# Optimization experiments

Measured on AMD Instinct MI355X. Metric: run time of the kernel, lower is better.

## Reference

```python
import jax, jax.numpy as jnp
import numpy as np

EPS = 1e-6

def _layernorm(x, g, b):
    m = jnp.mean(x, axis=-1, keepdims=True)
    v = jnp.var(x, axis=-1, keepdims=True)
    return (x - m) / jnp.sqrt(v + EPS) * g + b

def setup_inputs() -> dict:
    key = jax.random.key(0)
    ks = jax.random.split(key, 12)
    B, L, D, H = 2, 1024, 1024, 16
    s = 0.02  # weight init scale
    return {
        "query": jax.random.normal(ks[0], (B, L, D), jnp.float32),
        "pos_bias": jax.random.normal(ks[1], (H, L, L), jnp.float32) * 0.1,
        "postag_bias": jax.random.normal(ks[2], (B, H, L, L), jnp.float32) * 0.1,
        "lex_mask": jax.random.normal(ks[3], (B, L), jnp.float32) * 0.1,
        "mask": jax.random.randint(ks[4], (B, L), 0, 2).astype(jnp.int32),
        "Wq": jax.random.normal(ks[5], (D, D), jnp.float32) * s,
        "bq": jnp.zeros((D,), jnp.float32),
        "Wk": jax.random.normal(ks[6], (D, D), jnp.float32) * s,
        "bk": jnp.zeros((D,), jnp.float32),
        "Wv": jax.random.normal(ks[7], (D, D), jnp.float32) * s,
        "bv": jnp.zeros((D,), jnp.float32),
        "Wo": jax.random.normal(ks[8], (D, D), jnp.float32) * s,
        "bo": jnp.zeros((D,), jnp.float32),
        "gamma": jnp.ones((D,), jnp.float32),
        "beta": jnp.zeros((D,), jnp.float32),
    }

def reference(query, pos_bias, postag_bias, lex_mask, mask,
              Wq, bq, Wk, bk, Wv, bv, Wo, bo, gamma, beta):
    B, L, D = query.shape
    H = pos_bias.shape[0]
    dk = D // H
    scale = jnp.asarray(dk ** 0.5, query.dtype)

    residual = query
    context = query              # context=None path: set BEFORE pre-LN norm
    qn = _layernorm(query, gamma, beta)  # pre_ln=True applies only to query

    Q = (qn @ Wq.T + bq).reshape(B, L, H, dk)       # bqhd
    K = (context @ Wk.T + bk).reshape(B, L, H, dk)  # bkhd
    V = (context @ Wv.T + bv).reshape(B, L, H, dk)

    # (B,H,L,S) logits with all additive bias terms
    logits = jnp.einsum('bqhd,bkhd->bhqk', Q, K) / scale
    logits = logits + pos_bias[None]               # rel-pos bias (H,L,S)
    logits = logits + postag_bias                  # POS-tag bias (B,H,L,S)
    logits = logits + lex_mask[:, None, None, :]   # additive lexical mask
    logits = jnp.where(mask[:, None, None, :] == 0, -jnp.inf, logits)

    attn = jax.nn.softmax(logits, axis=-1)         # dropout inactive (eval)
    out = jnp.einsum('bhqk,bkhd->bqhd', attn, V).reshape(B, L, D)
    out = out @ Wo.T + bo
    out = out + residual
    return out, attn
```

## Files before the change

### kernel.cpp

```cpp
#include <hip/hip_runtime.h>
#include <hip/hip_bf16.h>
#include <math.h>

constexpr int B = 2, L = 1024, D = 1024, H = 16, DK = 64;
constexpr int M = B * L;
constexpr int DD = D * D;

typedef __attribute__((ext_vector_type(8))) short bf16x8;
typedef __attribute__((ext_vector_type(4))) float f32x4;

#define SB0() __builtin_amdgcn_sched_barrier(0)

__device__ inline unsigned short f2bf(float f) {
    __hip_bfloat16 h = __float2bfloat16(f);
    return __builtin_bit_cast(unsigned short, h);
}

__device__ inline void glds16(const void* g, void* l) {
    __builtin_amdgcn_global_load_lds((const __attribute__((address_space(1))) void*)g,
                                     (__attribute__((address_space(3))) void*)l,
                                     16, 0, 0);
}

__global__ __launch_bounds__(256) void ln2_kernel(const float* __restrict__ x,
                                                  const float* __restrict__ gamma,
                                                  const float* __restrict__ beta,
                                                  const float* __restrict__ lex,
                                                  const int* __restrict__ mask,
                                                  unsigned short* __restrict__ qn16,
                                                  unsigned short* __restrict__ q16,
                                                  float* __restrict__ lsmout) {
    int row = blockIdx.x;
    int t = threadIdx.x;
    if (t == 0) lsmout[row] = mask[row] ? lex[row] : -1e30f;
    const float4 v = ((const float4*)(x + (size_t)row * D))[t];
    float s  = v.x + v.y + v.z + v.w;
    float sq = v.x*v.x + v.y*v.y + v.z*v.z + v.w*v.w;
    #pragma unroll
    for (int m = 32; m >= 1; m >>= 1) {
        s  += __shfl_xor(s, m, 64);
        sq += __shfl_xor(sq, m, 64);
    }
    __shared__ float rs[4], rq[4];
    int wid = t >> 6;
    if ((t & 63) == 0) { rs[wid] = s; rq[wid] = sq; }
    __syncthreads();
    s  = rs[0] + rs[1] + rs[2] + rs[3];
    sq = rq[0] + rq[1] + rq[2] + rq[3];
    float mean = s * (1.0f / D);
    float var  = sq * (1.0f / D) - mean * mean;
    float rstd = rsqrtf(var + 1e-6f);
    float4 g  = ((const float4*)gamma)[t];
    float4 bb = ((const float4*)beta)[t];
    ushort4 on, oq;
    on.x = f2bf((v.x - mean) * rstd * g.x + bb.x);
    on.y = f2bf((v.y - mean) * rstd * g.y + bb.y);
    on.z = f2bf((v.z - mean) * rstd * g.z + bb.z);
    on.w = f2bf((v.w - mean) * rstd * g.w + bb.w);
    oq.x = f2bf(v.x); oq.y = f2bf(v.y); oq.z = f2bf(v.z); oq.w = f2bf(v.w);
    ((ushort4*)(qn16 + (size_t)row * D))[t] = on;
    ((ushort4*)(q16  + (size_t)row * D))[t] = oq;
}

__global__ __launch_bounds__(256) void wconv_kernel(const float* __restrict__ Wq,
                                                    const float* __restrict__ Wk,
                                                    const float* __restrict__ Wv,
                                                    const float* __restrict__ Wo,
                                                    unsigned short* __restrict__ out) {
    const float* src = (blockIdx.y == 0) ? Wq : (blockIdx.y == 1) ? Wk
                       : (blockIdx.y == 2) ? Wv : Wo;
    size_t i = (size_t)blockIdx.x * 256 + threadIdx.x;
    float4 v = ((const float4*)src)[i];
    ushort4 o;
    o.x = f2bf(v.x); o.y = f2bf(v.y); o.z = f2bf(v.z); o.w = f2bf(v.w);
    ((ushort4*)(out + (size_t)blockIdx.y * DD))[i] = o;
}

__global__ __launch_bounds__(256) void gemm_qkv(
        const unsigned short* __restrict__ qn16, const unsigned short* __restrict__ q16,
        const unsigned short* __restrict__ W,
        const float* __restrict__ bq, const float* __restrict__ bk,
        const float* __restrict__ bv,
        unsigned short* __restrict__ Qm, unsigned short* __restrict__ Km,
        unsigned short* __restrict__ Vm) {
    __shared__ __align__(16) unsigned short As[128 * 64];
    __shared__ __align__(16) unsigned short Ws[128 * 64];
    int t = threadIdx.x, lane = t & 63, w = t >> 6;
    int quad = lane >> 4, l15 = lane & 15;
    int nt = blockIdx.x;
    int bm = blockIdx.y * 128;
    const unsigned short* A = (nt < 8) ? qn16 : q16;
    const float* bias = (nt < 8) ? bq : ((nt < 16) ? bk : bv);
    unsigned short* Cout = (nt < 8) ? Qm : ((nt < 16) ? Km : Vm);
    int bn_local = (nt & 7) * 128;
    int wm = (w >> 1) * 64, wn = (w & 1) * 64;
    f32x4 acc[4][4] = {};
    for (int k0 = 0; k0 < D; k0 += 64) {
        __syncthreads();
        const unsigned short* ap = A + (size_t)(bm + w * 32) * D + k0;
        const unsigned short* wp = W + (size_t)(nt * 128 + w * 32) * D + k0;
        #pragma unroll
        for (int i = 0; i < 4; i++) {
            int c = i * 64 + lane;
            int r = c >> 3, g = (c & 7) ^ (r & 7);
            glds16(ap + (size_t)r * D + g * 8, &As[w * 2048 + i * 512]);
            glds16(wp + (size_t)r * D + g * 8, &Ws[w * 2048 + i * 512]);
        }
        __syncthreads();
        #pragma unroll
        for (int k2 = 0; k2 < 2; k2++) {
            bf16x8 av[4], bw[4];
            #pragma unroll
            for (int i = 0; i < 4; i++) {
                int r = wm + i * 16 + l15;
                av[i] = *(const bf16x8*)&As[r * 64 + (((quad + 4 * k2) ^ (r & 7)) * 8)];
            }
            #pragma unroll
            for (int j = 0; j < 4; j++) {
                int r = wn + j * 16 + l15;
                bw[j] = *(const bf16x8*)&Ws[r * 64 + (((quad + 4 * k2) ^ (r & 7)) * 8)];
            }
            #pragma unroll
            for (int i = 0; i < 4; i++)
                #pragma unroll
                for (int j = 0; j < 4; j++)
                    acc[i][j] = __builtin_amdgcn_mfma_f32_16x16x32_bf16(av[i], bw[j], acc[i][j], 0, 0, 0);
        }
    }
    #pragma unroll
    for (int j = 0; j < 4; j++) {
        int col = bn_local + wn + j * 16 + l15;
        float bcol = bias[col];
        #pragma unroll
        for (int i = 0; i < 4; i++)
            #pragma unroll
            for (int rg = 0; rg < 4; rg++) {
                int row = bm + wm + i * 16 + quad * 4 + rg;
                Cout[(size_t)row * D + col] = f2bf(acc[i][j][rg] + bcol);
            }
    }
}

__global__ __launch_bounds__(256) void vtrans_kernel(const unsigned short* __restrict__ Vm,
                                                     unsigned short* __restrict__ Vt) {
    __shared__ unsigned short sb[128 * 66];
    int t = threadIdx.x;
    int z = blockIdx.y;
    int b = z >> 4, h = z & 15;
    int s0 = blockIdx.x * 128;
    size_t base = (size_t)b * L * D + (size_t)h * 64;
    #pragma unroll
    for (int i = 0; i < 4; i++) {
        int idx = t + 256 * i;
        int r = idx >> 3, c8 = idx & 7;
        uint4 vv = *(const uint4*)&Vm[base + (size_t)(s0 + r) * D + c8 * 8];
        unsigned int* sp = (unsigned int*)&sb[r * 66 + c8 * 8];
        sp[0] = vv.x; sp[1] = vv.y; sp[2] = vv.z; sp[3] = vv.w;
    }
    __syncthreads();
    #pragma unroll
    for (int i = 0; i < 4; i++) {
        int idx = t + 256 * i;
        int d = idx >> 4, sc = idx & 15;
        unsigned short tmp[8];
        #pragma unroll
        for (int j = 0; j < 8; j++) tmp[j] = sb[(sc * 8 + j) * 66 + d];
        *(uint4*)&Vt[((size_t)z * 64 + d) * L + s0 + sc * 8] = *(uint4*)tmp;
    }
}

__global__ __launch_bounds__(256, 2) void attn_pv_kernel(
        const unsigned short* __restrict__ Qm, const unsigned short* __restrict__ Km,
        const unsigned short* __restrict__ Vt,
        const float* __restrict__ pos_bias, const float* __restrict__ postag,
        const float* __restrict__ lsm, float* __restrict__ attn_out,
        unsigned short* __restrict__ ctx16) {
    __shared__ __align__(16) unsigned short pool[32768];
    __shared__ __align__(16) unsigned short p_sh[16][136];
    __shared__ __align__(16) unsigned short q_sh[16][72];
    __shared__ float lsm_sh[1024];
    __shared__ float redA[16][4], redB[16][4];

    int t = threadIdx.x, lane = t & 63, w = t >> 6;
    int quad = lane >> 4, l15 = lane & 15;
    int qt = blockIdx.x & 63;
    int bh = blockIdx.x >> 6;
    int b = bh >> 4, h = bh & 15;
    int q0 = qt * 16;
    int q = q0 + l15;
    size_t base = (size_t)b * L * D + (size_t)h * DK;

    if (t < 128) {
        int r = t >> 3, c8 = t & 7;
        *(uint4*)&q_sh[r][c8 * 8] = *(const uint4*)&Qm[base + (size_t)(q0 + r) * D + c8 * 8];
    }
    ((float4*)lsm_sh)[t] = ((const float4*)(lsm + b * L))[t];
    __syncthreads();
    bf16x8 qb0 = *(const bf16x8*)&q_sh[l15][quad * 8];
    bf16x8 qb1 = *(const bf16x8*)&q_sh[l15][32 + quad * 8];

    const float* pbQ = pos_bias + ((size_t)h * L + q0) * L;
    const float* ptQ = postag + ((size_t)bh * L + q0) * L;

    f32x4 acc[16] = {};
    SB0();
    {
        const unsigned short* kpn = Km + base + (size_t)(w * 32) * D;
        #pragma unroll
        for (int i = 0; i < 4; i++) {
            int r = i * 8 + (lane >> 3);
            int g = (lane & 7) ^ (r & 7);
            glds16(kpn + (size_t)r * D + g * 8, &pool[w * 2048 + i * 512]);
        }
    }
    SB0();
    {
        int rb = lane >> 3;
        int gb = (lane & 7) ^ rb;
        #pragma unroll
        for (int i = 0; i < 2; i++) {
            glds16(pbQ + (size_t)(i * 8 + rb) * L + w * 32 + gb * 4,
                   &pool[16384 + w * 2048 + i * 512]);
            glds16(ptQ + (size_t)(i * 8 + rb) * L + w * 32 + gb * 4,
                   &pool[16384 + w * 2048 + 1024 + i * 512]);
        }
    }
    SB0();
    #pragma unroll
    for (int st = 0; st < 8; st++) {
        int bc = st & 1, bn = bc ^ 1;
        if (st < 7) {
            SB0();
            const unsigned short* kpn = Km + base + (size_t)((st + 1) * 128 + w * 32) * D;
            #pragma unroll
            for (int i = 0; i < 4; i++) {
                int r = i * 8 + (lane >> 3);
                int g = (lane & 7) ^ (r & 7);
                glds16(kpn + (size_t)r * D + g * 8, &pool[bn * 8192 + w * 2048 + i * 512]);
            }
            SB0();
            {
                int rb = lane >> 3;
                int gb = (lane & 7) ^ rb;
                #pragma unroll
                for (int i = 0; i < 2; i++) {
                    glds16(pbQ + (size_t)(i * 8 + rb) * L + (st + 1) * 128 + w * 32 + gb * 4,
                           &pool[16384 + bn * 8192 + w * 2048 + i * 512]);
                    glds16(ptQ + (size_t)(i * 8 + rb) * L + (st + 1) * 128 + w * 32 + gb * 4,
                           &pool[16384 + bn * 8192 + w * 2048 + 1024 + i * 512]);
                }
            }
            SB0();
            asm volatile("s_waitcnt vmcnt(8)" ::: "memory");
        } else {
            SB0();
            asm volatile("s_waitcnt vmcnt(0)" ::: "memory");
        }
        SB0();
        int r7 = l15 & 7;
        const unsigned short* kB = &pool[bc * 8192 + w * 2048];
        bf16x8 ka00 = *(const bf16x8*)&kB[l15 * 64 + ((quad ^ r7) * 8)];
        bf16x8 ka01 = *(const bf16x8*)&kB[l15 * 64 + (((quad + 4) ^ r7) * 8)];
        bf16x8 ka10 = *(const bf16x8*)&kB[(16 + l15) * 64 + ((quad ^ r7) * 8)];
        bf16x8 ka11 = *(const bf16x8*)&kB[(16 + l15) * 64 + (((quad + 4) ^ r7) * 8)];
        const float* pbL = (const float*)&pool[16384 + bc * 8192 + w * 2048];
        const float* ptL = (const float*)&pool[16384 + bc * 8192 + w * 2048 + 1024];
        float4 pb0 = *(const float4*)&pbL[l15 * 32 + ((quad ^ r7) * 4)];
        float4 pb1 = *(const float4*)&pbL[l15 * 32 + (((quad + 4) ^ r7) * 4)];
        float4 pt0 = *(const float4*)&ptL[l15 * 32 + ((quad ^ r7) * 4)];
        float4 pt1 = *(const float4*)&ptL[l15 * 32 + (((quad + 4) ^ r7) * 4)];
        int s_u0 = st * 128 + w * 32 + quad * 4;
        float4 l0 = *(const float4*)&lsm_sh[s_u0];
        float4 l1 = *(const float4*)&lsm_sh[s_u0 + 16];
        int ti0 = 2 * st, ti1 = ti0 + 1;
        acc[ti0] = __builtin_amdgcn_mfma_f32_16x16x32_bf16(ka00, qb0, acc[ti0], 0, 0, 0);
        acc[ti0] = __builtin_amdgcn_mfma_f32_16x16x32_bf16(ka01, qb1, acc[ti0], 0, 0, 0);
        acc[ti1] = __builtin_amdgcn_mfma_f32_16x16x32_bf16(ka10, qb0, acc[ti1], 0, 0, 0);
        acc[ti1] = __builtin_amdgcn_mfma_f32_16x16x32_bf16(ka11, qb1, acc[ti1], 0, 0, 0);
        acc[ti0][0] = acc[ti0][0] * 0.125f + (pb0.x + pt0.x + l0.x);
        acc[ti0][1] = acc[ti0][1] * 0.125f + (pb0.y + pt0.y + l0.y);
        acc[ti0][2] = acc[ti0][2] * 0.125f + (pb0.z + pt0.z + l0.z);
        acc[ti0][3] = acc[ti0][3] * 0.125f + (pb0.w + pt0.w + l0.w);
        acc[ti1][0] = acc[ti1][0] * 0.125f + (pb1.x + pt1.x + l1.x);
        acc[ti1][1] = acc[ti1][1] * 0.125f + (pb1.y + pt1.y + l1.y);
        acc[ti1][2] = acc[ti1][2] * 0.125f + (pb1.z + pt1.z + l1.z);
        acc[ti1][3] = acc[ti1][3] * 0.125f + (pb1.w + pt1.w + l1.w);
    }
    float mx = -1e30f;
    #pragma unroll
    for (int ti = 0; ti < 16; ti++)
        #pragma unroll
        for (int rg = 0; rg < 4; rg++) mx = fmaxf(mx, acc[ti][rg]);
    mx = fmaxf(mx, __shfl_xor(mx, 16, 64));
    mx = fmaxf(mx, __shfl_xor(mx, 32, 64));
    if (quad == 0) redA[l15][w] = mx;
    __syncthreads();
    mx = fmaxf(fmaxf(redA[l15][0], redA[l15][1]), fmaxf(redA[l15][2], redA[l15][3]));
    float sum = 0.f;
    #pragma unroll
    for (int ti = 0; ti < 16; ti++)
        #pragma unroll
        for (int rg = 0; rg < 4; rg++) {
            float e = __expf(acc[ti][rg] - mx);
            acc[ti][rg] = e;
            sum += e;
        }
    sum += __shfl_xor(sum, 16, 64);
    sum += __shfl_xor(sum, 32, 64);
    if (quad == 0) redB[l15][w] = sum;
    __syncthreads();
    float inv = 1.0f / (redB[l15][0] + redB[l15][1] + redB[l15][2] + redB[l15][3]);
    #pragma unroll
    for (int ti = 0; ti < 16; ti++) {
        int s0 = (ti >> 1) * 128 + w * 32 + (ti & 1) * 16 + quad * 4;
        float4 o;
        o.x = acc[ti][0] * inv; o.y = acc[ti][1] * inv;
        o.z = acc[ti][2] * inv; o.w = acc[ti][3] * inv;
        acc[ti][0] = o.x; acc[ti][1] = o.y; acc[ti][2] = o.z; acc[ti][3] = o.w;
        *(float4*)&attn_out[((size_t)bh * L + q) * L + s0] = o;
    }
    f32x4 cacc = {};
    const unsigned short* vbase = Vt + ((size_t)bh * 64 + w * 16) * L;
    SB0();
    #pragma unroll
    for (int i = 0; i < 4; i++) {
        int r = i * 4 + (lane >> 4);
        int g = (lane & 15) ^ (r & 7);
        glds16(vbase + (size_t)r * L + g * 8, &pool[w * 2048 + i * 512]);
    }
    SB0();
    #pragma unroll
    for (int st = 0; st < 8; st++) {
        int bc = st & 1;
        #pragma unroll
        for (int u = 0; u < 2; u++) {
            f32x4 p = acc[2 * st + u];
            ushort4 pu;
            pu.x = f2bf(p[0]); pu.y = f2bf(p[1]); pu.z = f2bf(p[2]); pu.w = f2bf(p[3]);
            *(ushort4*)&p_sh[l15][w * 32 + u * 16 + quad * 4] = pu;
        }
        if (st < 7) {
            SB0();
            #pragma unroll
            for (int i = 0; i < 4; i++) {
                int r = i * 4 + (lane >> 4);
                int g = (lane & 15) ^ (r & 7);
                glds16(vbase + (size_t)r * L + (st + 1) * 128 + g * 8,
                       &pool[(bc ^ 1) * 8192 + w * 2048 + i * 512]);
            }
            SB0();
            asm volatile("s_waitcnt vmcnt(4)" ::: "memory");
        } else {
            SB0();
            asm volatile("s_waitcnt vmcnt(0)" ::: "memory");
        }
        asm volatile("s_waitcnt lgkmcnt(0)" ::: "memory");
        SB0();
        __builtin_amdgcn_s_barrier();
        SB0();
        const unsigned short* vB = &pool[bc * 8192 + w * 2048];
        #pragma unroll
        for (int kk = 0; kk < 4; kk++) {
            bf16x8 vf = *(const bf16x8*)&vB[l15 * 128 + (((kk * 4 + quad) ^ (l15 & 7)) * 8)];
            bf16x8 pf = *(const bf16x8*)&p_sh[l15][kk * 32 + quad * 8];
            cacc = __builtin_amdgcn_mfma_f32_16x16x32_bf16(pf, vf, cacc, 0, 0, 0);
        }
        SB0();
        __builtin_amdgcn_s_barrier();
        SB0();
    }
    size_t cbase = ((size_t)b * L + q0) * D + (size_t)h * 64 + w * 16 + l15;
    #pragma unroll
    for (int rg = 0; rg < 4; rg++)
        ctx16[cbase + (size_t)(quad * 4 + rg) * D] = f2bf(cacc[rg]);
}

__global__ __launch_bounds__(256) void gemm_out(
        const unsigned short* __restrict__ A, const unsigned short* __restrict__ W,
        const float* __restrict__ bias, const float* __restrict__ res,
        float* __restrict__ C) {
    __shared__ __align__(16) unsigned short As[64 * 64];
    __shared__ __align__(16) unsigned short Ws[64 * 64];
    int t = threadIdx.x, lane = t & 63, w = t >> 6;
    int quad = lane >> 4, l15 = lane & 15;
    int bm = blockIdx.x * 64, bn = blockIdx.y * 64;
    int wm = (w >> 1) * 32, wn = (w & 1) * 32;
    f32x4 acc[2][2] = {};
    for (int k0 = 0; k0 < D; k0 += 64) {
        __syncthreads();
        const unsigned short* ap = A + (size_t)(bm + w * 16) * D + k0;
        const unsigned short* wp = W + (size_t)(bn + w * 16) * D + k0;
        #pragma unroll
        for (int i = 0; i < 2; i++) {
            int c = i * 64 + lane;
            int r = c >> 3, g = (c & 7) ^ (r & 7);
            glds16(ap + (size_t)r * D + g * 8, &As[w * 1024 + i * 512]);
            glds16(wp + (size_t)r * D + g * 8, &Ws[w * 1024 + i * 512]);
        }
        __syncthreads();
        #pragma unroll
        for (int k2 = 0; k2 < 2; k2++) {
            bf16x8 av[2], bw[2];
            #pragma unroll
            for (int i = 0; i < 2; i++) {
                int r = wm + i * 16 + l15;
                av[i] = *(const bf16x8*)&As[r * 64 + (((quad + 4 * k2) ^ (r & 7)) * 8)];
            }
            #pragma unroll
            for (int j = 0; j < 2; j++) {
                int r = wn + j * 16 + l15;
                bw[j] = *(const bf16x8*)&Ws[r * 64 + (((quad + 4 * k2) ^ (r & 7)) * 8)];
            }
            #pragma unroll
            for (int i = 0; i < 2; i++)
                #pragma unroll
                for (int j = 0; j < 2; j++)
                    acc[i][j] = __builtin_amdgcn_mfma_f32_16x16x32_bf16(av[i], bw[j], acc[i][j], 0, 0, 0);
        }
    }
    #pragma unroll
    for (int j = 0; j < 2; j++) {
        int col = bn + wn + j * 16 + l15;
        float bcol = bias[col];
        #pragma unroll
        for (int i = 0; i < 2; i++)
            #pragma unroll
            for (int rg = 0; rg < 4; rg++) {
                int row = bm + wm + i * 16 + quad * 4 + rg;
                C[(size_t)row * D + col] = acc[i][j][rg] + bcol + res[(size_t)row * D + col];
            }
    }
}

extern "C" void kernel_launch(void* const* d_in, const int* in_sizes, int n_in,
                              void* d_out, int out_size, void* d_ws, size_t ws_size,
                              hipStream_t stream) {
    (void)in_sizes; (void)n_in; (void)out_size; (void)ws_size;
    const float* query  = (const float*)d_in[0];
    const float* pos_b  = (const float*)d_in[1];
    const float* postag = (const float*)d_in[2];
    const float* lex    = (const float*)d_in[3];
    const int*   mask   = (const int*)d_in[4];
    const float* Wq = (const float*)d_in[5];
    const float* bq = (const float*)d_in[6];
    const float* Wk = (const float*)d_in[7];
    const float* bk = (const float*)d_in[8];
    const float* Wv = (const float*)d_in[9];
    const float* bv = (const float*)d_in[10];
    const float* Wo = (const float*)d_in[11];
    const float* bo = (const float*)d_in[12];
    const float* gamma = (const float*)d_in[13];
    const float* beta  = (const float*)d_in[14];

    float* out  = (float*)d_out;
    float* attn = out + (size_t)B * L * D;

    unsigned short* ws16 = (unsigned short*)d_ws;
    const size_t NE = (size_t)M * D;
    unsigned short* qn16  = ws16;
    unsigned short* q16   = ws16 + NE;
    unsigned short* W16   = ws16 + 2 * NE;
    unsigned short* Qm16  = W16 + 4 * (size_t)DD;
    unsigned short* Km16  = Qm16 + NE;
    unsigned short* Vm16  = Km16 + NE;
    unsigned short* Vt16  = Vm16 + NE;
    unsigned short* ctx16 = Vt16 + NE;
    float* lsm = (float*)(ctx16 + NE);

    ln2_kernel<<<M, 256, 0, stream>>>(query, gamma, beta, lex, mask, qn16, q16, lsm);
    wconv_kernel<<<dim3(DD / 1024, 4), 256, 0, stream>>>(Wq, Wk, Wv, Wo, W16);
    gemm_qkv<<<dim3(24, 16), 256, 0, stream>>>(qn16, q16, W16, bq, bk, bv,
                                               Qm16, Km16, Vm16);
    vtrans_kernel<<<dim3(8, 32), 256, 0, stream>>>(Vm16, Vt16);
    attn_pv_kernel<<<B * H * (L / 16), 256, 0, stream>>>(Qm16, Km16, Vt16,
                                                         pos_b, postag, lsm,
                                                         attn, ctx16);
    gemm_out<<<dim3(32, 16), 256, 0, stream>>>(ctx16, W16 + 3 * (size_t)DD, bo, query, out);
}
```

Before: 402.2 us.

## Double-buffer GEMM tiles and restructure attention bias loads for higher occupancy

Both the QKV and output GEMMs now double-buffer their LDS tiles, so the next k-tile's global-to-LDS loads overlap the MFMAs on the current tile, with explicit vmcnt waits and barriers. The attention kernel stops staging pos_bias and postag through LDS and instead register-prefetches them directly, which cuts its shared memory. It also aliases p_sh, lsm and q_sh into one region so that launch bounds can be raised from 2 to 4 blocks per CU. Each wave now owns a contiguous 256-key slice, so P stores to p_sh are done by one wave per step, which adds an extra barrier and serialises that write.

```diff
diff --git a/kernel.cpp b/kernel.cpp
--- a/kernel.cpp
+++ b/kernel.cpp
@@ -83,8 +83,8 @@
         const float* __restrict__ bv,
         unsigned short* __restrict__ Qm, unsigned short* __restrict__ Km,
         unsigned short* __restrict__ Vm) {
-    __shared__ __align__(16) unsigned short As[128 * 64];
-    __shared__ __align__(16) unsigned short Ws[128 * 64];
+    __shared__ __align__(16) unsigned short As[2][8192];
+    __shared__ __align__(16) unsigned short Ws[2][8192];
     int t = threadIdx.x, lane = t & 63, w = t >> 6;
     int quad = lane >> 4, l15 = lane & 15;
     int nt = blockIdx.x;
@@ -94,31 +94,52 @@
     unsigned short* Cout = (nt < 8) ? Qm : ((nt < 16) ? Km : Vm);
     int bn_local = (nt & 7) * 128;
     int wm = (w >> 1) * 64, wn = (w & 1) * 64;
+    const unsigned short* ap0 = A + (size_t)(bm + w * 32) * D;
+    const unsigned short* wp0 = W + (size_t)(nt * 128 + w * 32) * D;
     f32x4 acc[4][4] = {};
-    for (int k0 = 0; k0 < D; k0 += 64) {
-        __syncthreads();
-        const unsigned short* ap = A + (size_t)(bm + w * 32) * D + k0;
-        const unsigned short* wp = W + (size_t)(nt * 128 + w * 32) * D + k0;
-        #pragma unroll
-        for (int i = 0; i < 4; i++) {
-            int c = i * 64 + lane;
-            int r = c >> 3, g = (c & 7) ^ (r & 7);
-            glds16(ap + (size_t)r * D + g * 8, &As[w * 2048 + i * 512]);
-            glds16(wp + (size_t)r * D + g * 8, &Ws[w * 2048 + i * 512]);
-        }
-        __syncthreads();
+
+    #define QKV_STAGE(kt, c)                                                  \
+        {                                                                     \
+            const unsigned short* ap = ap0 + (kt) * 64;                       \
+            const unsigned short* wp = wp0 + (kt) * 64;                       \
+            _Pragma("unroll")                                                 \
+            for (int i = 0; i < 4; i++) {                                     \
+                int cc = i * 64 + lane;                                       \
+                int r = cc >> 3, g = (cc & 7) ^ (r & 7);                      \
+                glds16(ap + (size_t)r * D + g * 8, &As[c][w * 2048 + i * 512]);\
+                glds16(wp + (size_t)r * D + g * 8, &Ws[c][w * 2048 + i * 512]);\
+            }                                                                 \
+        }
+
+    SB0();
+    QKV_STAGE(0, 0);
+    SB0();
+    for (int kt = 0; kt < 16; kt++) {
+        int c = kt & 1;
+        if (kt < 15) {
+            SB0();
+            QKV_STAGE(kt + 1, c ^ 1);
+            SB0();
+            asm volatile("s_waitcnt vmcnt(8)" ::: "memory");
+        } else {
+            SB0();
+            asm volatile("s_waitcnt vmcnt(0)" ::: "memory");
+        }
+        SB0();
+        __builtin_amdgcn_s_barrier();
+        SB0();
         #pragma unroll
         for (int k2 = 0; k2 < 2; k2++) {
             bf16x8 av[4], bw[4];
             #pragma unroll
             for (int i = 0; i < 4; i++) {
                 int r = wm + i * 16 + l15;
-                av[i] = *(const bf16x8*)&As[r * 64 + (((quad + 4 * k2) ^ (r & 7)) * 8)];
+                av[i] = *(const bf16x8*)&As[c][r * 64 + (((quad + 4 * k2) ^ (r & 7)) * 8)];
             }
             #pragma unroll
             for (int j = 0; j < 4; j++) {
                 int r = wn + j * 16 + l15;
-                bw[j] = *(const bf16x8*)&Ws[r * 64 + (((quad + 4 * k2) ^ (r & 7)) * 8)];
+                bw[j] = *(const bf16x8*)&Ws[c][r * 64 + (((quad + 4 * k2) ^ (r & 7)) * 8)];
             }
             #pragma unroll
             for (int i = 0; i < 4; i++)
@@ -126,6 +147,9 @@
                 for (int j = 0; j < 4; j++)
                     acc[i][j] = __builtin_amdgcn_mfma_f32_16x16x32_bf16(av[i], bw[j], acc[i][j], 0, 0, 0);
         }
+        SB0();
+        __builtin_amdgcn_s_barrier();
+        SB0();
     }
     #pragma unroll
     for (int j = 0; j < 4; j++) {
@@ -139,6 +163,7 @@
                 Cout[(size_t)row * D + col] = f2bf(acc[i][j][rg] + bcol);
             }
     }
+    #undef QKV_STAGE
 }
 
 __global__ __launch_bounds__(256) void vtrans_kernel(const unsigned short* __restrict__ Vm,
@@ -169,17 +194,19 @@
     }
 }
 
-__global__ __launch_bounds__(256, 2) void attn_pv_kernel(
+__global__ __launch_bounds__(256, 4) void attn_pv_kernel(
         const unsigned short* __restrict__ Qm, const unsigned short* __restrict__ Km,
         const unsigned short* __restrict__ Vt,
         const float* __restrict__ pos_bias, const float* __restrict__ postag,
         const float* __restrict__ lsm, float* __restrict__ attn_out,
         unsigned short* __restrict__ ctx16) {
-    __shared__ __align__(16) unsigned short pool[32768];
-    __shared__ __align__(16) unsigned short p_sh[16][136];
-    __shared__ __align__(16) unsigned short q_sh[16][72];
-    __shared__ float lsm_sh[1024];
-    __shared__ float redA[16][4], redB[16][4];
+    __shared__ __align__(16) unsigned short pool[16384];
+    __shared__ __align__(16) unsigned short reg2[3456];
+    float* lsm_sh = (float*)reg2;
+    unsigned short (*q_sh)[72] = (unsigned short(*)[72])(reg2 + 2048);
+    float (*redA)[4] = (float(*)[4])(reg2 + 3200);
+    float (*redB)[4] = (float(*)[4])(reg2 + 3328);
+    unsigned short (*p_sh)[136] = (unsigned short(*)[136])reg2;
 
     int t = threadIdx.x, lane = t & 63, w = t >> 6;
     int quad = lane >> 4, l15 = lane & 15;
@@ -199,57 +226,46 @@
     bf16x8 qb0 = *(const bf16x8*)&q_sh[l15][quad * 8];
     bf16x8 qb1 = *(const bf16x8*)&q_sh[l15][32 + quad * 8];
 
-    const float* pbQ = pos_bias + ((size_t)h * L + q0) * L;
-    const float* ptQ = postag + ((size_t)bh * L + q0) * L;
+    const float* pbp = pos_bias + ((size_t)h * L + q) * L;
+    const float* ptp = postag + ((size_t)bh * L + q) * L;
+    const unsigned short* kbase = Km + base + (size_t)(w * 256) * D;
+    int squad = w * 256 + quad * 4;
+
+    SB0();
+    #pragma unroll
+    for (int i = 0; i < 4; i++) {
+        int r = i * 8 + (lane >> 3);
+        int g = (lane & 7) ^ (r & 7);
+        glds16(kbase + (size_t)r * D + g * 8, &pool[w * 2048 + i * 512]);
+    }
+    SB0();
+    float4 pbc0 = *(const float4*)(pbp + squad);
+    float4 pbc1 = *(const float4*)(pbp + squad + 16);
+    float4 ptc0 = *(const float4*)(ptp + squad);
+    float4 ptc1 = *(const float4*)(ptp + squad + 16);
+    SB0();
 
     f32x4 acc[16] = {};
-    SB0();
-    {
-        const unsigned short* kpn = Km + base + (size_t)(w * 32) * D;
-        #pragma unroll
-        for (int i = 0; i < 4; i++) {
-            int r = i * 8 + (lane >> 3);
-            int g = (lane & 7) ^ (r & 7);
-            glds16(kpn + (size_t)r * D + g * 8, &pool[w * 2048 + i * 512]);
-        }
-    }
-    SB0();
-    {
-        int rb = lane >> 3;
-        int gb = (lane & 7) ^ rb;
-        #pragma unroll
-        for (int i = 0; i < 2; i++) {
-            glds16(pbQ + (size_t)(i * 8 + rb) * L + w * 32 + gb * 4,
-                   &pool[16384 + w * 2048 + i * 512]);
-            glds16(ptQ + (size_t)(i * 8 + rb) * L + w * 32 + gb * 4,
-                   &pool[16384 + w * 2048 + 1024 + i * 512]);
-        }
-    }
-    SB0();
     #pragma unroll
     for (int st = 0; st < 8; st++) {
-        int bc = st & 1, bn = bc ^ 1;
+        int bc = st & 1;
+        float4 pbn0, pbn1, ptn0, ptn1;
         if (st < 7) {
             SB0();
-            const unsigned short* kpn = Km + base + (size_t)((st + 1) * 128 + w * 32) * D;
+            const unsigned short* kpn = kbase + (size_t)((st + 1) * 32) * D;
             #pragma unroll
             for (int i = 0; i < 4; i++) {
                 int r = i * 8 + (lane >> 3);
                 int g = (lane & 7) ^ (r & 7);
-                glds16(kpn + (size_t)r * D + g * 8, &pool[bn * 8192 + w * 2048 + i * 512]);
-            }
-            SB0();
-            {
-                int rb = lane >> 3;
-                int gb = (lane & 7) ^ rb;
-                #pragma unroll
-                for (int i = 0; i < 2; i++) {
-                    glds16(pbQ + (size_t)(i * 8 + rb) * L + (st + 1) * 128 + w * 32 + gb * 4,
-                           &pool[16384 + bn * 8192 + w * 2048 + i * 512]);
-                    glds16(ptQ + (size_t)(i * 8 + rb) * L + (st + 1) * 128 + w * 32 + gb * 4,
-                           &pool[16384 + bn * 8192 + w * 2048 + 1024 + i * 512]);
-                }
-            }
+                glds16(kpn + (size_t)r * D + g * 8,
+                       &pool[(bc ^ 1) * 8192 + w * 2048 + i * 512]);
+            }
+            SB0();
+            int sn = squad + (st + 1) * 32;
+            pbn0 = *(const float4*)(pbp + sn);
+            pbn1 = *(const float4*)(pbp + sn + 16);
+            ptn0 = *(const float4*)(ptp + sn);
+            ptn1 = *(const float4*)(ptp + sn + 16);
             SB0();
             asm volatile("s_waitcnt vmcnt(8)" ::: "memory");
         } else {
@@ -263,28 +279,22 @@
         bf16x8 ka01 = *(const bf16x8*)&kB[l15 * 64 + (((quad + 4) ^ r7) * 8)];
         bf16x8 ka10 = *(const bf16x8*)&kB[(16 + l15) * 64 + ((quad ^ r7) * 8)];
         bf16x8 ka11 = *(const bf16x8*)&kB[(16 + l15) * 64 + (((quad + 4) ^ r7) * 8)];
-        const float* pbL = (const float*)&pool[16384 + bc * 8192 + w * 2048];
-        const float* ptL = (const float*)&pool[16384 + bc * 8192 + w * 2048 + 1024];
-        float4 pb0 = *(const float4*)&pbL[l15 * 32 + ((quad ^ r7) * 4)];
-        float4 pb1 = *(const float4*)&pbL[l15 * 32 + (((quad + 4) ^ r7) * 4)];
-        float4 pt0 = *(const float4*)&ptL[l15 * 32 + ((quad ^ r7) * 4)];
-        float4 pt1 = *(const float4*)&ptL[l15 * 32 + (((quad + 4) ^ r7) * 4)];
-        int s_u0 = st * 128 + w * 32 + quad * 4;
-        float4 l0 = *(const float4*)&lsm_sh[s_u0];
-        float4 l1 = *(const float4*)&lsm_sh[s_u0 + 16];
+        float4 l0 = *(const float4*)&lsm_sh[squad + st * 32];
+        float4 l1 = *(const float4*)&lsm_sh[squad + st * 32 + 16];
         int ti0 = 2 * st, ti1 = ti0 + 1;
         acc[ti0] = __builtin_amdgcn_mfma_f32_16x16x32_bf16(ka00, qb0, acc[ti0], 0, 0, 0);
         acc[ti0] = __builtin_amdgcn_mfma_f32_16x16x32_bf16(ka01, qb1, acc[ti0], 0, 0, 0);
         acc[ti1] = __builtin_amdgcn_mfma_f32_16x16x32_bf16(ka10, qb0, acc[ti1], 0, 0, 0);
         acc[ti1] = __builtin_amdgcn_mfma_f32_16x16x32_bf16(ka11, qb1, acc[ti1], 0, 0, 0);
-        acc[ti0][0] = acc[ti0][0] * 0.125f + (pb0.x + pt0.x + l0.x);
-        acc[ti0][1] = acc[ti0][1] * 0.125f + (pb0.y + pt0.y + l0.y);
-        acc[ti0][2] = acc[ti0][2] * 0.125f + (pb0.z + pt0.z + l0.z);
-        acc[ti0][3] = acc[ti0][3] * 0.125f + (pb0.w + pt0.w + l0.w);
-        acc[ti1][0] = acc[ti1][0] * 0.125f + (pb1.x + pt1.x + l1.x);
-        acc[ti1][1] = acc[ti1][1] * 0.125f + (pb1.y + pt1.y + l1.y);
-        acc[ti1][2] = acc[ti1][2] * 0.125f + (pb1.z + pt1.z + l1.z);
-        acc[ti1][3] = acc[ti1][3] * 0.125f + (pb1.w + pt1.w + l1.w);
+        acc[ti0][0] = acc[ti0][0] * 0.125f + (pbc0.x + ptc0.x + l0.x);
+        acc[ti0][1] = acc[ti0][1] * 0.125f + (pbc0.y + ptc0.y + l0.y);
+        acc[ti0][2] = acc[ti0][2] * 0.125f + (pbc0.z + ptc0.z + l0.z);
+        acc[ti0][3] = acc[ti0][3] * 0.125f + (pbc0.w + ptc0.w + l0.w);
+        acc[ti1][0] = acc[ti1][0] * 0.125f + (pbc1.x + ptc1.x + l1.x);
+        acc[ti1][1] = acc[ti1][1] * 0.125f + (pbc1.y + ptc1.y + l1.y);
+        acc[ti1][2] = acc[ti1][2] * 0.125f + (pbc1.z + ptc1.z + l1.z);
+        acc[ti1][3] = acc[ti1][3] * 0.125f + (pbc1.w + ptc1.w + l1.w);
+        if (st < 7) { pbc0 = pbn0; pbc1 = pbn1; ptc0 = ptn0; ptc1 = ptn1; }
     }
     float mx = -1e30f;
     #pragma unroll
@@ -312,13 +322,14 @@
     float inv = 1.0f / (redB[l15][0] + redB[l15][1] + redB[l15][2] + redB[l15][3]);
     #pragma unroll
     for (int ti = 0; ti < 16; ti++) {
-        int s0 = (ti >> 1) * 128 + w * 32 + (ti & 1) * 16 + quad * 4;
+        int s0 = w * 256 + (ti >> 1) * 32 + (ti & 1) * 16 + quad * 4;
         float4 o;
         o.x = acc[ti][0] * inv; o.y = acc[ti][1] * inv;
         o.z = acc[ti][2] * inv; o.w = acc[ti][3] * inv;
         acc[ti][0] = o.x; acc[ti][1] = o.y; acc[ti][2] = o.z; acc[ti][3] = o.w;
         *(float4*)&attn_out[((size_t)bh * L + q) * L + s0] = o;
     }
+    __syncthreads();
     f32x4 cacc = {};
     const unsigned short* vbase = Vt + ((size_t)bh * 64 + w * 16) * L;
     SB0();
@@ -332,13 +343,6 @@
     #pragma unroll
     for (int st = 0; st < 8; st++) {
         int bc = st & 1;
-        #pragma unroll
-        for (int u = 0; u < 2; u++) {
-            f32x4 p = acc[2 * st + u];
-            ushort4 pu;
-            pu.x = f2bf(p[0]); pu.y = f2bf(p[1]); pu.z = f2bf(p[2]); pu.w = f2bf(p[3]);
-            *(ushort4*)&p_sh[l15][w * 32 + u * 16 + quad * 4] = pu;
-        }
         if (st < 7) {
             SB0();
             #pragma unroll
@@ -349,12 +353,20 @@
                        &pool[(bc ^ 1) * 8192 + w * 2048 + i * 512]);
             }
             SB0();
-            asm volatile("s_waitcnt vmcnt(4)" ::: "memory");
-        } else {
-            SB0();
-            asm volatile("s_waitcnt vmcnt(0)" ::: "memory");
+        }
+        if (w == (st >> 1)) {
+            #pragma unroll
+            for (int u = 0; u < 8; u++) {
+                f32x4 p = acc[(st & 1) * 8 + u];
+                ushort4 pu;
+                pu.x = f2bf(p[0]); pu.y = f2bf(p[1]); pu.z = f2bf(p[2]); pu.w = f2bf(p[3]);
+                *(ushort4*)&p_sh[l15][u * 16 + quad * 4] = pu;
+            }
         }
         asm volatile("s_waitcnt lgkmcnt(0)" ::: "memory");
+        SB0();
+        if (st < 7) asm volatile("s_waitcnt vmcnt(4)" ::: "memory");
+        else        asm volatile("s_waitcnt vmcnt(0)" ::: "memory");
         SB0();
         __builtin_amdgcn_s_barrier();
         SB0();
@@ -379,37 +391,58 @@
         const unsigned short* __restrict__ A, const unsigned short* __restrict__ W,
         const float* __restrict__ bias, const float* __restrict__ res,
         float* __restrict__ C) {
-    __shared__ __align__(16) unsigned short As[64 * 64];
-    __shared__ __align__(16) unsigned short Ws[64 * 64];
+    __shared__ __align__(16) unsigned short As[2][4096];
+    __shared__ __align__(16) unsigned short Ws[2][4096];
     int t = threadIdx.x, lane = t & 63, w = t >> 6;
     int quad = lane >> 4, l15 = lane & 15;
     int bm = blockIdx.x * 64, bn = blockIdx.y * 64;
     int wm = (w >> 1) * 32, wn = (w & 1) * 32;
+    const unsigned short* ap0 = A + (size_t)(bm + w * 16) * D;
+    const unsigned short* wp0 = W + (size_t)(bn + w * 16) * D;
     f32x4 acc[2][2] = {};
-    for (int k0 = 0; k0 < D; k0 += 64) {
-        __syncthreads();
-        const unsigned short* ap = A + (size_t)(bm + w * 16) * D + k0;
-        const unsigned short* wp = W + (size_t)(bn + w * 16) * D + k0;
-        #pragma unroll
-        for (int i = 0; i < 2; i++) {
-            int c = i * 64 + lane;
-            int r = c >> 3, g = (c & 7) ^ (r & 7);
-            glds16(ap + (size_t)r * D + g * 8, &As[w * 1024 + i * 512]);
-            glds16(wp + (size_t)r * D + g * 8, &Ws[w * 1024 + i * 512]);
-        }
-        __syncthreads();
+
+    #define OUT_STAGE(kt, c)                                                  \
+        {                                                                     \
+            const unsigned short* ap = ap0 + (kt) * 64;                       \
+            const unsigned short* wp = wp0 + (kt) * 64;                       \
+            _Pragma("unroll")                                                 \
+            for (int i = 0; i < 2; i++) {                                     \
+                int cc = i * 64 + lane;                                       \
+                int r = cc >> 3, g = (cc & 7) ^ (r & 7);                      \
+                glds16(ap + (size_t)r * D + g * 8, &As[c][w * 1024 + i * 512]);\
+                glds16(wp + (size_t)r * D + g * 8, &Ws[c][w * 1024 + i * 512]);\
+            }                                                                 \
+        }
+
+    SB0();
+    OUT_STAGE(0, 0);
+    SB0();
+    for (int kt = 0; kt < 16; kt++) {
+        int c = kt & 1;
+        if (kt < 15) {
+            SB0();
+            OUT_STAGE(kt + 1, c ^ 1);
+            SB0();
+            asm volatile("s_waitcnt vmcnt(4)" ::: "memory");
+        } else {
+            SB0();
+            asm volatile("s_waitcnt vmcnt(0)" ::: "memory");
+        }
+        SB0();
+        __builtin_amdgcn_s_barrier();
+        SB0();
         #pragma unroll
         for (int k2 = 0; k2 < 2; k2++) {
             bf16x8 av[2], bw[2];
             #pragma unroll
             for (int i = 0; i < 2; i++) {
                 int r = wm + i * 16 + l15;
-                av[i] = *(const bf16x8*)&As[r * 64 + (((quad + 4 * k2) ^ (r & 7)) * 8)];
+                av[i] = *(const bf16x8*)&As[c][r * 64 + (((quad + 4 * k2) ^ (r & 7)) * 8)];
             }
             #pragma unroll
             for (int j = 0; j < 2; j++) {
                 int r = wn + j * 16 + l15;
-                bw[j] = *(const bf16x8*)&Ws[r * 64 + (((quad + 4 * k2) ^ (r & 7)) * 8)];
+                bw[j] = *(const bf16x8*)&Ws[c][r * 64 + (((quad + 4 * k2) ^ (r & 7)) * 8)];
             }
             #pragma unroll
             for (int i = 0; i < 2; i++)
@@ -417,6 +450,9 @@
                 for (int j = 0; j < 2; j++)
                     acc[i][j] = __builtin_amdgcn_mfma_f32_16x16x32_bf16(av[i], bw[j], acc[i][j], 0, 0, 0);
         }
+        SB0();
+        __builtin_amdgcn_s_barrier();
+        SB0();
     }
     #pragma unroll
     for (int j = 0; j < 2; j++) {
@@ -430,6 +466,7 @@
                 C[(size_t)row * D + col] = acc[i][j][rg] + bcol + res[(size_t)row * D + col];
             }
     }
+    #undef OUT_STAGE
 }
 
 extern "C" void kernel_launch(void* const* d_in, const int* in_sizes, int n_in,
```

Measured after the change: 407.8 us. No clear change (+1.4%).
